# Performance work log

Hardware: AMD Instinct MI355X
Metric: run time of the kernel (lower is better)

The kernel has to match this reference:

```python
import jax, jax.numpy as jnp
import numpy as np

T, H, I, E, TOPK = 4096, 2880, 2880, 16, 4
EPS = 1e-5
ALPHA = 1.702


def setup_inputs() -> dict:
    key = jax.random.key(0)
    ks = jax.random.split(key, 8)
    s = 0.02
    return {
        "x": jax.random.normal(ks[0], (T, H), dtype=jnp.float32),
        "norm_w": jnp.ones((H,), dtype=jnp.float32),
        "gate_w": jax.random.normal(ks[1], (E, H), dtype=jnp.float32) * s,
        "gate_b": jax.random.normal(ks[2], (E,), dtype=jnp.float32) * s,
        "w1": jax.random.normal(ks[3], (E, 2 * I, H), dtype=jnp.float32) * s,  # fused gate_up
        "b1": jax.random.normal(ks[4], (E, 2 * I), dtype=jnp.float32) * s,
        "w2": jax.random.normal(ks[5], (E, H, I), dtype=jnp.float32) * s,      # down proj
        "b2": jax.random.normal(ks[6], (E, H), dtype=jnp.float32) * s,
    }


def _rmsnorm(x, w, eps=EPS):
    var = jnp.mean(x * x, axis=-1, keepdims=True)
    return x * jax.lax.rsqrt(var + eps) * w


def _swiglu(gu):
    glu, lin = jnp.split(gu, 2, axis=-1)
    return glu * jax.nn.sigmoid(ALPHA * glu) * (lin + 1.0)


def reference(x, norm_w, gate_w, gate_b, w1, b1, w2, b2):
    t = _rmsnorm(x, norm_w)                       # [T, H]
    logits = t @ gate_w.T + gate_b                # [T, E]
    # Renormalize routing: top-k of logits, softmax over the k selected logits
    vals, idx = jax.lax.top_k(logits, TOPK)       # [T, k]
    wts = jax.nn.softmax(vals, axis=-1)           # [T, k]
    combine = jnp.zeros((t.shape[0], E), dtype=t.dtype)
    combine = combine.at[jnp.arange(t.shape[0])[:, None], idx].set(wts)  # [T, E]
    out = jnp.zeros_like(x)
    for e in range(E):                            # small fixed expert loop
        gu = t @ w1[e].T + b1[e]                  # [T, 2I]
        y = _swiglu(gu) @ w2[e].T + b2[e]         # [T, H]
        out = out + combine[:, e:e + 1] * y
    return x + out
```

## Files before the change

### kernel.cpp

```cpp
#include <hip/hip_runtime.h>
#include <hip/hip_bf16.h>
#include <math.h>
#include <stdint.h>

#define T_TOK 4096
#define H_DIM 2880
#define E_NUM 16
#define ALPHA 1.702f
#define EPS_RMS 1e-5f

#define PADM 192
#define BK 32
#define NK (H_DIM / BK)
#define MAX_RT 104
#define NCT1 30
#define NCT2 15
#define G1 (MAX_RT * NCT1)
#define G2 (MAX_RT * NCT2)
#define ABUF 12288
#define BBUF 12288
#define BOFF 36864

typedef __attribute__((ext_vector_type(8))) short short8;
typedef __attribute__((ext_vector_type(4))) float f32x4;

__device__ __forceinline__ unsigned short f2bf(float f) {
  unsigned u = __float_as_uint(f);
  return (unsigned short)((u + 0x7fffu + ((u >> 16) & 1u)) >> 16);
}
__device__ __forceinline__ unsigned cpk(float a, float b) {
  unsigned r;
  asm("v_cvt_pk_bf16_f32 %0, %1, %2" : "=v"(r) : "v"(a), "v"(b));
  return r;
}
__device__ __forceinline__ void gl_lds16(const void* g, unsigned char* lds_dst) {
  __builtin_amdgcn_global_load_lds(
      (const __attribute__((address_space(1))) void*)g,
      (__attribute__((address_space(3))) void*)lds_dst, 16, 0, 0);
}
#define ENDSTEP() do {                                           \
    asm volatile("s_waitcnt lgkmcnt(0)" ::: "memory");           \
    __builtin_amdgcn_s_barrier();                                \
    __builtin_amdgcn_sched_barrier(0);                           \
  } while (0)

__global__ __launch_bounds__(256) void k_norm_gate(
    const float* __restrict__ x, const float* __restrict__ norm_w,
    const float* __restrict__ gate_w, const float* __restrict__ gate_b,
    float* __restrict__ out, unsigned short* __restrict__ t_out,
    int* __restrict__ topk_id, float* __restrict__ topk_w,
    int* __restrict__ counts)
{
  int t = blockIdx.x, tid = threadIdx.x;
  const float4* xr = (const float4*)(x + (size_t)t * H_DIM);
  float4* outr = (float4*)(out + (size_t)t * H_DIM);
  float4 xa[3];
  float ss = 0.f;
  int j = 0;
  for (int i = tid; i < 720; i += 256, j++) {
    float4 v = xr[i]; xa[j] = v; outr[i] = v;
    ss += v.x * v.x + v.y * v.y + v.z * v.z + v.w * v.w;
  }
#pragma unroll
  for (int o = 1; o < 64; o <<= 1) ss += __shfl_xor(ss, o, 64);
  __shared__ float red[4];
  if ((tid & 63) == 0) red[tid >> 6] = ss;
  __syncthreads();
  float rs = rsqrtf((red[0] + red[1] + red[2] + red[3]) * (1.f / H_DIM) + EPS_RMS);

  float part[16];
#pragma unroll
  for (int q = 0; q < 16; q++) part[q] = 0.f;
  j = 0;
  for (int i = tid; i < 720; i += 256, j++) {
    float4 v = xa[j];
    float4 w = ((const float4*)norm_w)[i];
    float t0 = v.x * rs * w.x, t1 = v.y * rs * w.y;
    float t2 = v.z * rs * w.z, t3 = v.w * rs * w.w;
    ushort4 b; b.x = f2bf(t0); b.y = f2bf(t1); b.z = f2bf(t2); b.w = f2bf(t3);
    ((ushort4*)(t_out + (size_t)t * H_DIM))[i] = b;
#pragma unroll
    for (int q = 0; q < 16; q++) {
      float4 g = ((const float4*)(gate_w + (size_t)q * H_DIM))[i];
      part[q] += t0 * g.x + t1 * g.y + t2 * g.z + t3 * g.w;
    }
  }
  __shared__ float lg[4][16];
#pragma unroll
  for (int q = 0; q < 16; q++) {
    float p = part[q];
#pragma unroll
    for (int o = 1; o < 64; o <<= 1) p += __shfl_xor(p, o, 64);
    if ((tid & 63) == 0) lg[tid >> 6][q] = p;
  }
  __syncthreads();
  if (tid == 0) {
    float logit[16];
    for (int q = 0; q < 16; q++)
      logit[q] = lg[0][q] + lg[1][q] + lg[2][q] + lg[3][q] + gate_b[q];
    unsigned used = 0; int idx[4]; float val[4];
    for (int k = 0; k < 4; k++) {
      float best = -3.4e38f; int bi = 0;
      for (int q = 0; q < 16; q++)
        if (!((used >> q) & 1u) && logit[q] > best) { best = logit[q]; bi = q; }
      used |= 1u << bi; idx[k] = bi; val[k] = best;
    }
    float s0 = 0.f, w4[4];
    for (int k = 0; k < 4; k++) { w4[k] = expf(val[k] - val[0]); s0 += w4[k]; }
    for (int k = 0; k < 4; k++) {
      topk_id[t * 4 + k] = idx[k];
      topk_w[t * 4 + k] = w4[k] / s0;
      atomicAdd(&counts[idx[k]], 1);
    }
  }
}

__global__ void k_offsets(const int* __restrict__ counts, int* __restrict__ d_off) {
  if (threadIdx.x == 0) {
    int acc = 0;
    for (int q = 0; q < 16; q++) {
      d_off[q] = acc;
      acc += ((counts[q] + PADM - 1) / PADM) * PADM;
    }
    d_off[16] = acc;
  }
}

__global__ __launch_bounds__(256) void k_fill(
    const int* __restrict__ topk_id, const float* __restrict__ topk_w,
    const int* __restrict__ counts, const int* __restrict__ d_off,
    int* __restrict__ perm_tok, float* __restrict__ perm_w)
{
  int e = blockIdx.x;
  int base = d_off[e], pe = d_off[e + 1] - base, cnt = counts[e];
  int tid = threadIdx.x, lane = tid & 63, wv = tid >> 6;
  __shared__ int wsum[4];
  int pos = 0;
  for (int c0 = 0; c0 < T_TOK; c0 += 256) {
    int tok = c0 + tid;
    int4 ids = ((const int4*)topk_id)[tok];
    int flag = 0, slot = 0;
    if (ids.x == e) { flag = 1; slot = 0; }
    else if (ids.y == e) { flag = 1; slot = 1; }
    else if (ids.z == e) { flag = 1; slot = 2; }
    else if (ids.w == e) { flag = 1; slot = 3; }
    unsigned long long b = __ballot(flag);
    int wprefix = __popcll(b & ((1ULL << lane) - 1ULL));
    if (lane == 0) wsum[wv] = __popcll(b);
    __syncthreads();
    int woff = 0;
    for (int i = 0; i < wv; i++) woff += wsum[i];
    int tot = wsum[0] + wsum[1] + wsum[2] + wsum[3];
    if (flag) {
      int p = base + pos + woff + wprefix;
      perm_tok[p] = tok;
      perm_w[p] = topk_w[tok * 4 + slot];
    }
    pos += tot;
    __syncthreads();
  }
  for (int i = cnt + tid; i < pe; i += 256) {
    perm_tok[base + i] = 0;
    perm_w[base + i] = 0.f;
  }
}

#define STAGE_A(abuf, ktn) do {                                               \
  _Pragma("unroll")                                                           \
  for (int i = 0; i < 3; i++)                                                 \
    gl_lds16(aptr[i] + (size_t)(ktn) * BK, lds + (abuf) * ABUF + adst[i]);    \
} while (0)

#define LOAD_B(ktn) do {                                                      \
  _Pragma("unroll")                                                           \
  for (int j = 0; j < 3; j++) {                                               \
    bv[j][0] = bptr[j][(ktn) * 8];                                            \
    bv[j][1] = bptr[j][(ktn) * 8 + 1];                                        \
  }                                                                           \
} while (0)

#define PACK_B(bbuf) do {                                                     \
  _Pragma("unroll")                                                           \
  for (int j = 0; j < 3; j++) {                                               \
    uint4 p;                                                                  \
    p.x = cpk(bv[j][0].x, bv[j][0].y); p.y = cpk(bv[j][0].z, bv[j][0].w);     \
    p.z = cpk(bv[j][1].x, bv[j][1].y); p.w = cpk(bv[j][1].z, bv[j][1].w);     \
    *(uint4*)(lds + BOFF + (bbuf) * BBUF + bdst[j]) = p;                      \
  }                                                                           \
} while (0)

#define COMPUTE(abuf, bbuf) do {                                              \
  const unsigned char* Abase = lds + (abuf) * ABUF + abase_off;               \
  const unsigned char* Bbase = lds + BOFF + (bbuf) * BBUF + bbase_off;        \
  short8 a0 = *(const short8*)(Abase);                                        \
  short8 a1 = *(const short8*)(Abase + 1024);                                 \
  short8 a2 = *(const short8*)(Abase + 2048);                                 \
  __builtin_amdgcn_s_setprio(1);                                              \
  _Pragma("unroll")                                                           \
  for (int n = 0; n < 12; n++) {                                              \
    short8 b = *(const short8*)(Bbase + n * 1024);                            \
    acc[0][n] = __builtin_amdgcn_mfma_f32_16x16x32_bf16(a0, b, acc[0][n], 0, 0, 0); \
    acc[1][n] = __builtin_amdgcn_mfma_f32_16x16x32_bf16(a1, b, acc[1][n], 0, 0, 0); \
    acc[2][n] = __builtin_amdgcn_mfma_f32_16x16x32_bf16(a2, b, acc[2][n], 0, 0, 0); \
  }                                                                           \
  __builtin_amdgcn_s_setprio(0);                                              \
} while (0)

#define GEMM_PIPE() do {                                                      \
  STAGE_A(0, 0); STAGE_A(1, 1); LOAD_B(0);                                    \
  PACK_B(0);                \
  ENDSTEP();                                                                  \
  int ca = 0;                                                                 \
  _Pragma("unroll 1")                                                         \
  for (int u = 0; u < NK / 2; u++) {                                          \
    int kt = 2 * u;                                                           \
    int ca1 = ca + 1; if (ca1 >= 3) ca1 -= 3;                                 \
    int ca2 = ca + 2; if (ca2 >= 3) ca2 -= 3;                                 \
    if (kt + 1 < NK) LOAD_B(kt + 1);                                          \
    if (kt + 2 < NK) STAGE_A(ca2, kt + 2);                                    \
    COMPUTE(ca, 0);                                                           \
    if (kt + 1 < NK) PACK_B(1);                                               \
    ENDSTEP();                                                                \
    if (kt + 2 < NK) LOAD_B(kt + 2);                                          \
    if (kt + 3 < NK) STAGE_A(ca, kt + 3);                                     \
    COMPUTE(ca1, 1);                                                          \
    if (kt + 2 < NK) PACK_B(0);                                               \
    ENDSTEP();                                                                \
    ca = ca2;                                                                 \
  }                                                                           \
} while (0)

__global__ __launch_bounds__(256, 2) void k_gemm1(
    const unsigned short* __restrict__ t_bf16,
    const float* __restrict__ w1, const float* __restrict__ b1,
    const int* __restrict__ perm_tok, const int* __restrict__ d_off,
    unsigned short* __restrict__ act)
{
  __shared__ __align__(16) unsigned char lds[3 * ABUF + 2 * BBUF];
  const int total = d_off[16];
  int bid = blockIdx.x;
  int wg = (bid & 7) * (G1 / 8) + (bid >> 3);
  int ct = wg / MAX_RT, rt = wg % MAX_RT;
  int rowbase = rt * PADM;
  if (rowbase >= total) return;
  int e = 0;
#pragma unroll
  for (int q = 0; q < E_NUM; q++) if (d_off[q + 1] <= rowbase) e = q + 1;

  int tid = threadIdx.x, lane = tid & 63, wv = tid >> 6;
  int lr = lane & 15, ch = lane >> 4;
  unsigned swz16 = (unsigned)((ch ^ ((lr >> 1) & 3)) << 4);
  unsigned abase_off = (unsigned)(wv * 3072 + lr * 64) + swz16;
  unsigned bbase_off = (unsigned)(lr * 64) + swz16;

  const unsigned short* aptr[3]; unsigned adst[3];
#pragma unroll
  for (int i = 0; i < 3; i++) {
    int cl = tid + 256 * i;
    int r = cl >> 2, c = cl & 3;
    int tok = perm_tok[rowbase + r];
    aptr[i] = t_bf16 + (size_t)tok * H_DIM + ((c ^ ((r >> 1) & 3)) * 8);
    adst[i] = (unsigned)cl * 16;
  }
  const float4* bptr[3]; unsigned bdst[3];
#pragma unroll
  for (int j = 0; j < 3; j++) {
    int idx = tid + 256 * j;
    int rr = idx >> 2, c = idx & 3;
    size_t grow = (size_t)e * (2 * H_DIM) +
                  (rr < 96 ? (size_t)(ct * 96 + rr) : (size_t)(H_DIM + ct * 96 + (rr - 96)));
    bptr[j] = (const float4*)(w1 + grow * H_DIM) + c * 2;
    bdst[j] = (unsigned)(rr * 64 + ((c ^ ((rr >> 1) & 3)) << 4));
  }

  f32x4 zero = {0.f, 0.f, 0.f, 0.f};
  f32x4 acc[3][12];
#pragma unroll
  for (int m = 0; m < 3; m++)
#pragma unroll
    for (int n = 0; n < 12; n++) acc[m][n] = zero;
  float4 bv[3][2];

  GEMM_PIPE();

  int rq = lane >> 4;
#pragma unroll
  for (int m = 0; m < 3; m++) {
    int row0 = rowbase + wv * 48 + m * 16 + rq * 4;
#pragma unroll
    for (int n = 0; n < 6; n++) {
      int col = ct * 96 + n * 16 + lr;
      float bg = b1[(size_t)e * (2 * H_DIM) + col];
      float bl = b1[(size_t)e * (2 * H_DIM) + H_DIM + col];
#pragma unroll
      for (int j = 0; j < 4; j++) {
        float g = acc[m][n][j] + bg;
        float l = acc[m][n + 6][j] + bl;
        float s = 1.f / (1.f + __expf(-ALPHA * g));
        act[(size_t)(row0 + j) * H_DIM + col] = f2bf(g * s * (l + 1.f));
      }
    }
  }
}

__global__ __launch_bounds__(256, 2) void k_gemm2(
    const unsigned short* __restrict__ act,
    const float* __restrict__ w2, const float* __restrict__ b2,
    const int* __restrict__ perm_tok, const float* __restrict__ perm_w,
    const int* __restrict__ d_off,
    float* __restrict__ out)
{
  __shared__ __align__(16) unsigned char lds[3 * ABUF + 2 * BBUF];
  __shared__ int stok[PADM]; __shared__ float swt[PADM];
  const int total = d_off[16];
  int bid = blockIdx.x;
  int wg = (bid & 7) * (G2 / 8) + (bid >> 3);
  int ct = wg / MAX_RT, rt = wg % MAX_RT;
  int rowbase = rt * PADM;
  if (rowbase >= total) return;
  int e = 0;
#pragma unroll
  for (int q = 0; q < E_NUM; q++) if (d_off[q + 1] <= rowbase) e = q + 1;

  int tid = threadIdx.x, lane = tid & 63, wv = tid >> 6;
  int lr = lane & 15, ch = lane >> 4;
  unsigned swz16 = (unsigned)((ch ^ ((lr >> 1) & 3)) << 4);
  unsigned abase_off = (unsigned)(wv * 3072 + lr * 64) + swz16;
  unsigned bbase_off = (unsigned)(lr * 64) + swz16;

  if (tid < PADM) { stok[tid] = perm_tok[rowbase + tid]; swt[tid] = perm_w[rowbase + tid]; }

  const unsigned short* aptr[3]; unsigned adst[3];
#pragma unroll
  for (int i = 0; i < 3; i++) {
    int cl = tid + 256 * i;
    int r = cl >> 2, c = cl & 3;
    aptr[i] = act + (size_t)(rowbase + r) * H_DIM + ((c ^ ((r >> 1) & 3)) * 8);
    adst[i] = (unsigned)cl * 16;
  }
  const float4* bptr[3]; unsigned bdst[3];
#pragma unroll
  for (int j = 0; j < 3; j++) {
    int idx = tid + 256 * j;
    int rr = idx >> 2, c = idx & 3;
    size_t grow = (size_t)e * H_DIM + (size_t)(ct * 192 + rr);
    bptr[j] = (const float4*)(w2 + grow * H_DIM) + c * 2;
    bdst[j] = (unsigned)(rr * 64 + ((c ^ ((rr >> 1) & 3)) << 4));
  }

  f32x4 zero = {0.f, 0.f, 0.f, 0.f};
  f32x4 acc[3][12];
#pragma unroll
  for (int m = 0; m < 3; m++)
#pragma unroll
    for (int n = 0; n < 12; n++) acc[m][n] = zero;
  float4 bv[3][2];

  GEMM_PIPE();

  int rq = lane >> 4;
#pragma unroll
  for (int m = 0; m < 3; m++) {
    int rl0 = wv * 48 + m * 16 + rq * 4;
#pragma unroll
    for (int n = 0; n < 12; n++) {
      int col = ct * 192 + n * 16 + lr;
      float b2v = b2[(size_t)e * H_DIM + col];
#pragma unroll
      for (int j = 0; j < 4; j++) {
        int rl = rl0 + j;
        float w = swt[rl];
        if (w != 0.f)
          atomicAdd(out + (size_t)stok[rl] * H_DIM + col, (acc[m][n][j] + b2v) * w);
      }
    }
  }
}

extern "C" void kernel_launch(void* const* d_in, const int* in_sizes, int n_in,
                              void* d_out, int out_size, void* d_ws, size_t ws_size,
                              hipStream_t stream)
{
  const float* x      = (const float*)d_in[0];
  const float* norm_w = (const float*)d_in[1];
  const float* gate_w = (const float*)d_in[2];
  const float* gate_b = (const float*)d_in[3];
  const float* w1     = (const float*)d_in[4];
  const float* b1     = (const float*)d_in[5];
  const float* w2     = (const float*)d_in[6];
  const float* b2     = (const float*)d_in[7];
  float* out = (float*)d_out;
  char* ws = (char*)d_ws;

  unsigned short* t_bf16  = (unsigned short*)(ws);
  unsigned short* act     = (unsigned short*)(ws + 23592960);
  int*            topk_id = (int*)(ws + 138608640);
  float*          topk_w  = (float*)(ws + 138674176);
  int*            perm_tk = (int*)(ws + 138739712);
  float*          perm_w  = (float*)(ws + 138819584);
  int*            counts  = (int*)(ws + 138899456);
  int*            d_off   = (int*)(ws + 138899520);

  hipMemsetAsync(counts, 0, 64, stream);
  hipLaunchKernelGGL(k_norm_gate, dim3(T_TOK), dim3(256), 0, stream,
                     x, norm_w, gate_w, gate_b, out, t_bf16, topk_id, topk_w, counts);
  hipLaunchKernelGGL(k_offsets, dim3(1), dim3(64), 0, stream, counts, d_off);
  hipLaunchKernelGGL(k_fill, dim3(16), dim3(256), 0, stream,
                     topk_id, topk_w, counts, d_off, perm_tk, perm_w);
  hipLaunchKernelGGL(k_gemm1, dim3(G1), dim3(256), 0, stream,
                     t_bf16, w1, b1, perm_tk, d_off, act);
  hipLaunchKernelGGL(k_gemm2, dim3(G2), dim3(256), 0, stream,
                     act, w2, b2, perm_tk, perm_w, d_off, out);
}
```

Measured before the change: 1.573 ms.

## Triple-buffer B tile in LDS and deepen weight prefetch pipeline

Restructures the GEMM main loop so the B (weight) tile gets three LDS buffers like A, unrolled by three steps. Global B loads are now issued two k-steps ahead, and a sched_barrier separates the MFMA compute from the bf16 pack/store. The aim is to hide more of the fp32 weight-load latency behind the MFMAs. In exchange it uses more LDS per block (five to six 12 KB buffers), which may limit occupancy, and keeps B registers live longer.

After: 5.945 ms. 278% more time.

```diff
diff --git a/kernel.cpp b/kernel.cpp
--- a/kernel.cpp
+++ b/kernel.cpp
@@ -189,9 +189,9 @@
   }                                                                           \
 } while (0)
 
-#define COMPUTE(abuf, bbuf) do {                                              \
-  const unsigned char* Abase = lds + (abuf) * ABUF + abase_off;               \
-  const unsigned char* Bbase = lds + BOFF + (bbuf) * BBUF + bbase_off;        \
+#define COMPUTE(cb) do {                                                      \
+  const unsigned char* Abase = lds + (cb) * ABUF + abase_off;                 \
+  const unsigned char* Bbase = lds + BOFF + (cb) * BBUF + bbase_off;          \
   short8 a0 = *(const short8*)(Abase);                                        \
   short8 a1 = *(const short8*)(Abase + 1024);                                 \
   short8 a2 = *(const short8*)(Abase + 2048);                                 \
@@ -206,27 +206,28 @@
   __builtin_amdgcn_s_setprio(0);                                              \
 } while (0)
 
+#define GEMM_STEP(kt, CB, PB) do {                                            \
+    if ((kt) + 2 < NK) STAGE_A(PB, (kt) + 2);                                 \
+    COMPUTE(CB);                                                              \
+    __builtin_amdgcn_sched_barrier(0);                                        \
+    if ((kt) + 2 < NK) PACK_B(PB);                                            \
+    else asm volatile("s_waitcnt vmcnt(0)" ::: "memory");                     \
+    if ((kt) + 3 < NK) LOAD_B((kt) + 3);                                      \
+    ENDSTEP();                                                                \
+  } while (0)
+
 #define GEMM_PIPE() do {                                                      \
-  STAGE_A(0, 0); STAGE_A(1, 1); LOAD_B(0);                                    \
-  PACK_B(0);                \
+  STAGE_A(0, 0); STAGE_A(1, 1);                                               \
+  LOAD_B(0); PACK_B(0);                                                       \
+  LOAD_B(1); PACK_B(1);     \
+  LOAD_B(2);                             \
   ENDSTEP();                                                                  \
-  int ca = 0;                                                                 \
   _Pragma("unroll 1")                                                         \
-  for (int u = 0; u < NK / 2; u++) {                                          \
-    int kt = 2 * u;                                                           \
-    int ca1 = ca + 1; if (ca1 >= 3) ca1 -= 3;                                 \
-    int ca2 = ca + 2; if (ca2 >= 3) ca2 -= 3;                                 \
-    if (kt + 1 < NK) LOAD_B(kt + 1);                                          \
-    if (kt + 2 < NK) STAGE_A(ca2, kt + 2);                                    \
-    COMPUTE(ca, 0);                                                           \
-    if (kt + 1 < NK) PACK_B(1);                                               \
-    ENDSTEP();                                                                \
-    if (kt + 2 < NK) LOAD_B(kt + 2);                                          \
-    if (kt + 3 < NK) STAGE_A(ca, kt + 3);                                     \
-    COMPUTE(ca1, 1);                                                          \
-    if (kt + 2 < NK) PACK_B(0);                                               \
-    ENDSTEP();                                                                \
-    ca = ca2;                                                                 \
+  for (int u = 0; u < NK / 3; u++) {                                          \
+    int kt = 3 * u;                                                           \
+    GEMM_STEP(kt,     0, 2);                                                  \
+    GEMM_STEP(kt + 1, 1, 0);                                                  \
+    GEMM_STEP(kt + 2, 2, 1);                                                  \
   }                                                                           \
 } while (0)
 
@@ -236,7 +237,7 @@
     const int* __restrict__ perm_tok, const int* __restrict__ d_off,
     unsigned short* __restrict__ act)
 {
-  __shared__ __align__(16) unsigned char lds[3 * ABUF + 2 * BBUF];
+  __shared__ __align__(16) unsigned char lds[3 * ABUF + 3 * BBUF];
   const int total = d_off[16];
   int bid = blockIdx.x;
   int wg = (bid & 7) * (G1 / 8) + (bid >> 3);
@@ -310,7 +311,7 @@
     const int* __restrict__ d_off,
     float* __restrict__ out)
 {
-  __shared__ __align__(16) unsigned char lds[3 * ABUF + 2 * BBUF];
+  __shared__ __align__(16) unsigned char lds[3 * ABUF + 3 * BBUF];
   __shared__ int stok[PADM]; __shared__ float swt[PADM];
   const int total = d_off[16];
   int bid = blockIdx.x;
```

## Pre-convert expert weights to bf16 and use async LDS-staged GEMMs when workspace allows

Applied to the files above, without the earlier changes.

Adds a conversion kernel that writes w1 and w2 to bf16 in the workspace before each expert GEMM. New GEMM kernels stage both A and B tiles into LDS asynchronously in a three-buffer pipeline, with a 2x2 wave tiling over 6x3 or 6x6 fragments. This removes the per-thread fp32 weight loads and register packing. The cost is an extra full pass over the fp32 weights, writing 2-byte copies, on every call. The new path runs only if the workspace is large enough; otherwise the old kernels run, with slightly reordered staging.

After: 2.858 ms. +81.7%, slower.

```diff
diff --git a/kernel.cpp b/kernel.cpp
--- a/kernel.cpp
+++ b/kernel.cpp
@@ -165,6 +165,21 @@
   }
 }
 
+__global__ __launch_bounds__(256) void k_cvt(
+    const float* __restrict__ src, unsigned short* __restrict__ dst, int n8)
+{
+  int i = blockIdx.x * 256 + threadIdx.x;
+  int stride = gridDim.x * 256;
+  for (; i < n8; i += stride) {
+    float4 a = ((const float4*)src)[2 * i];
+    float4 b = ((const float4*)src)[2 * i + 1];
+    uint4 o;
+    o.x = cpk(a.x, a.y); o.y = cpk(a.z, a.w);
+    o.z = cpk(b.x, b.y); o.w = cpk(b.z, b.w);
+    ((uint4*)dst)[i] = o;
+  }
+}
+
 #define STAGE_A(abuf, ktn) do {                                               \
   _Pragma("unroll")                                                           \
   for (int i = 0; i < 3; i++)                                                 \
@@ -206,9 +221,17 @@
   __builtin_amdgcn_s_setprio(0);                                              \
 } while (0)
 
-#define GEMM_PIPE() do {                                                      \
+#define GEMM_STEP_F(kt, CB, PB) do {                                          \
+    if ((kt) + 1 < NK) LOAD_B((kt) + 1);                                      \
+    if ((kt) + 2 < NK) STAGE_A(PB, (kt) + 2);                                 \
+    COMPUTE(CB, (kt) & 1);                                                    \
+    if ((kt) + 1 < NK) PACK_B(((kt) + 1) & 1);                                \
+    ENDSTEP();                                                                \
+  } while (0)
+
+#define GEMM_PIPE_F() do {                                                    \
   STAGE_A(0, 0); STAGE_A(1, 1); LOAD_B(0);                                    \
-  PACK_B(0);                \
+  PACK_B(0);                                                                  \
   ENDSTEP();                                                                  \
   int ca = 0;                                                                 \
   _Pragma("unroll 1")                                                         \
@@ -216,13 +239,13 @@
     int kt = 2 * u;                                                           \
     int ca1 = ca + 1; if (ca1 >= 3) ca1 -= 3;                                 \
     int ca2 = ca + 2; if (ca2 >= 3) ca2 -= 3;                                 \
+    if (kt + 2 < NK) STAGE_A(ca2, kt + 2);                                    \
     if (kt + 1 < NK) LOAD_B(kt + 1);                                          \
-    if (kt + 2 < NK) STAGE_A(ca2, kt + 2);                                    \
     COMPUTE(ca, 0);                                                           \
     if (kt + 1 < NK) PACK_B(1);                                               \
     ENDSTEP();                                                                \
+    if (kt + 3 < NK) STAGE_A(ca, kt + 3);                                     \
     if (kt + 2 < NK) LOAD_B(kt + 2);                                          \
-    if (kt + 3 < NK) STAGE_A(ca, kt + 3);                                     \
     COMPUTE(ca1, 1);                                                          \
     if (kt + 2 < NK) PACK_B(0);                                               \
     ENDSTEP();                                                                \
@@ -230,7 +253,7 @@
   }                                                                           \
 } while (0)
 
-__global__ __launch_bounds__(256, 2) void k_gemm1(
+__global__ __launch_bounds__(256, 2) void k_gemm1_f(
     const unsigned short* __restrict__ t_bf16,
     const float* __restrict__ w1, const float* __restrict__ b1,
     const int* __restrict__ perm_tok, const int* __restrict__ d_off,
@@ -281,7 +304,7 @@
     for (int n = 0; n < 12; n++) acc[m][n] = zero;
   float4 bv[3][2];
 
-  GEMM_PIPE();
+  GEMM_PIPE_F();
 
   int rq = lane >> 4;
 #pragma unroll
@@ -303,7 +326,7 @@
   }
 }
 
-__global__ __launch_bounds__(256, 2) void k_gemm2(
+__global__ __launch_bounds__(256, 2) void k_gemm2_f(
     const unsigned short* __restrict__ act,
     const float* __restrict__ w2, const float* __restrict__ b2,
     const int* __restrict__ perm_tok, const float* __restrict__ perm_w,
@@ -356,7 +379,7 @@
     for (int n = 0; n < 12; n++) acc[m][n] = zero;
   float4 bv[3][2];
 
-  GEMM_PIPE();
+  GEMM_PIPE_F();
 
   int rq = lane >> 4;
 #pragma unroll
@@ -372,6 +395,211 @@
         float w = swt[rl];
         if (w != 0.f)
           atomicAdd(out + (size_t)stok[rl] * H_DIM + col, (acc[m][n][j] + b2v) * w);
+      }
+    }
+  }
+}
+
+#define STAGE_BW(bbuf, ktn) do {                                              \
+  _Pragma("unroll")                                                           \
+  for (int i = 0; i < 3; i++)                                                 \
+    gl_lds16(bpt[i] + (size_t)(ktn) * BK, lds + BOFF + (bbuf) * BBUF + adst[i]); \
+} while (0)
+
+#define WWAIT(full) do {                                                      \
+    if (full) asm volatile("s_waitcnt vmcnt(6)" ::: "memory");                \
+    else      asm volatile("s_waitcnt vmcnt(0)" ::: "memory");                \
+    __builtin_amdgcn_sched_barrier(0);                                        \
+    __builtin_amdgcn_s_barrier();                                             \
+    __builtin_amdgcn_sched_barrier(0);                                        \
+  } while (0)
+
+#define WSTEP(kt, CB, SB, COMP) do {                                          \
+    if ((kt) + 2 < NK) { STAGE_A(SB, (kt) + 2); STAGE_BW(SB, (kt) + 2); }     \
+    COMP(CB);                                                                 \
+    if ((kt) + 1 < NK) WWAIT((kt) + 2 < NK);                                  \
+  } while (0)
+
+#define WPIPE(COMP) do {                                                      \
+  STAGE_A(0, 0); STAGE_BW(0, 0);                                              \
+  STAGE_A(1, 1); STAGE_BW(1, 1);                                              \
+  WWAIT(1);                                                                   \
+  _Pragma("unroll 1")                                                         \
+  for (int u = 0; u < NK / 3; u++) {                                          \
+    int kt = 3 * u;                                                           \
+    WSTEP(kt,     0, 2, COMP);                                                \
+    WSTEP(kt + 1, 1, 0, COMP);                                                \
+    WSTEP(kt + 2, 2, 1, COMP);                                                \
+  }                                                                           \
+} while (0)
+
+#define COMP_G1(cb) do {                                                      \
+  const unsigned char* Ab = lds + (cb) * ABUF;                                \
+  const unsigned char* Bb = lds + BOFF + (cb) * BBUF;                         \
+  short8 a_[6];                                                               \
+  _Pragma("unroll")                                                           \
+  for (int mf = 0; mf < 6; mf++) a_[mf] = *(const short8*)(Ab + abase + mf * 1024); \
+  __builtin_amdgcn_s_setprio(1);                                              \
+  _Pragma("unroll")                                                           \
+  for (int nf = 0; nf < 3; nf++) {                                            \
+    short8 bg = *(const short8*)(Bb + bgbase + nf * 1024);                    \
+    short8 bl = *(const short8*)(Bb + blbase + nf * 1024);                    \
+    _Pragma("unroll")                                                         \
+    for (int mf = 0; mf < 6; mf++) {                                          \
+      accg[mf][nf] = __builtin_amdgcn_mfma_f32_16x16x32_bf16(a_[mf], bg, accg[mf][nf], 0, 0, 0); \
+      accl[mf][nf] = __builtin_amdgcn_mfma_f32_16x16x32_bf16(a_[mf], bl, accl[mf][nf], 0, 0, 0); \
+    }                                                                         \
+  }                                                                           \
+  __builtin_amdgcn_s_setprio(0);                                              \
+} while (0)
+
+#define COMP_G2(cb) do {                                                      \
+  const unsigned char* Ab = lds + (cb) * ABUF;                                \
+  const unsigned char* Bb = lds + BOFF + (cb) * BBUF;                         \
+  short8 a_[6];                                                               \
+  _Pragma("unroll")                                                           \
+  for (int mf = 0; mf < 6; mf++) a_[mf] = *(const short8*)(Ab + abase + mf * 1024); \
+  __builtin_amdgcn_s_setprio(1);                                              \
+  _Pragma("unroll")                                                           \
+  for (int nf = 0; nf < 6; nf++) {                                            \
+    short8 b = *(const short8*)(Bb + bbase + nf * 1024);                      \
+    _Pragma("unroll")                                                         \
+    for (int mf = 0; mf < 6; mf++)                                            \
+      acc[mf][nf] = __builtin_amdgcn_mfma_f32_16x16x32_bf16(a_[mf], b, acc[mf][nf], 0, 0, 0); \
+  }                                                                           \
+  __builtin_amdgcn_s_setprio(0);                                              \
+} while (0)
+
+__global__ __launch_bounds__(256, 2) void k_gemm1_w(
+    const unsigned short* __restrict__ t_bf16,
+    const unsigned short* __restrict__ w1b, const float* __restrict__ b1,
+    const int* __restrict__ perm_tok, const int* __restrict__ d_off,
+    unsigned short* __restrict__ act)
+{
+  __shared__ __align__(16) unsigned char lds[3 * ABUF + 3 * BBUF];
+  const int total = d_off[16];
+  int bid = blockIdx.x;
+  int wg = (bid & 7) * (G1 / 8) + (bid >> 3);
+  int ct = wg / MAX_RT, rt = wg % MAX_RT;
+  int rowbase = rt * PADM;
+  if (rowbase >= total) return;
+  int e = 0;
+#pragma unroll
+  for (int q = 0; q < E_NUM; q++) if (d_off[q + 1] <= rowbase) e = q + 1;
+
+  int tid = threadIdx.x, lane = tid & 63, wv = tid >> 6;
+  int wr = wv & 1, wc = wv >> 1;
+  int lr = lane & 15, ch = lane >> 4;
+  unsigned swz16 = (unsigned)((ch ^ ((lr >> 1) & 3)) << 4);
+  unsigned abase  = (unsigned)((wr * 96 + lr) * 64) + swz16;
+  unsigned bgbase = (unsigned)((wc * 48 + lr) * 64) + swz16;
+  unsigned blbase = bgbase + 96 * 64;
+
+  const unsigned short* aptr[3]; const unsigned short* bpt[3]; unsigned adst[3];
+#pragma unroll
+  for (int i = 0; i < 3; i++) {
+    int cl = tid + 256 * i;
+    int r = cl >> 2, c = cl & 3;
+    int cs = (c ^ ((r >> 1) & 3)) * 8;
+    int tok = perm_tok[rowbase + r];
+    aptr[i] = t_bf16 + (size_t)tok * H_DIM + cs;
+    size_t grow = (size_t)e * (2 * H_DIM) +
+                  (r < 96 ? (size_t)(ct * 96 + r) : (size_t)(H_DIM + ct * 96 + (r - 96)));
+    bpt[i] = w1b + grow * H_DIM + cs;
+    adst[i] = (unsigned)cl * 16;
+  }
+
+  f32x4 zero = {0.f, 0.f, 0.f, 0.f};
+  f32x4 accg[6][3], accl[6][3];
+#pragma unroll
+  for (int m = 0; m < 6; m++)
+#pragma unroll
+    for (int n = 0; n < 3; n++) { accg[m][n] = zero; accl[m][n] = zero; }
+
+  WPIPE(COMP_G1);
+
+  int rq = lane >> 4;
+#pragma unroll
+  for (int mf = 0; mf < 6; mf++) {
+    int row0 = rowbase + wr * 96 + mf * 16 + rq * 4;
+#pragma unroll
+    for (int nf = 0; nf < 3; nf++) {
+      int col = ct * 96 + wc * 48 + nf * 16 + lr;
+      float bg = b1[(size_t)e * (2 * H_DIM) + col];
+      float bl = b1[(size_t)e * (2 * H_DIM) + H_DIM + col];
+#pragma unroll
+      for (int j = 0; j < 4; j++) {
+        float g = accg[mf][nf][j] + bg;
+        float l = accl[mf][nf][j] + bl;
+        float s = 1.f / (1.f + __expf(-ALPHA * g));
+        act[(size_t)(row0 + j) * H_DIM + col] = f2bf(g * s * (l + 1.f));
+      }
+    }
+  }
+}
+
+__global__ __launch_bounds__(256, 2) void k_gemm2_w(
+    const unsigned short* __restrict__ act,
+    const unsigned short* __restrict__ w2b, const float* __restrict__ b2,
+    const int* __restrict__ perm_tok, const float* __restrict__ perm_w,
+    const int* __restrict__ d_off,
+    float* __restrict__ out)
+{
+  __shared__ __align__(16) unsigned char lds[3 * ABUF + 3 * BBUF];
+  __shared__ int stok[PADM]; __shared__ float swt[PADM];
+  const int total = d_off[16];
+  int bid = blockIdx.x;
+  int wg = (bid & 7) * (G2 / 8) + (bid >> 3);
+  int ct = wg / MAX_RT, rt = wg % MAX_RT;
+  int rowbase = rt * PADM;
+  if (rowbase >= total) return;
+  int e = 0;
+#pragma unroll
+  for (int q = 0; q < E_NUM; q++) if (d_off[q + 1] <= rowbase) e = q + 1;
+
+  int tid = threadIdx.x, lane = tid & 63, wv = tid >> 6;
+  int wr = wv & 1, wc = wv >> 1;
+  int lr = lane & 15, ch = lane >> 4;
+  unsigned swz16 = (unsigned)((ch ^ ((lr >> 1) & 3)) << 4);
+  unsigned abase = (unsigned)((wr * 96 + lr) * 64) + swz16;
+  unsigned bbase = (unsigned)((wc * 96 + lr) * 64) + swz16;
+
+  if (tid < PADM) { stok[tid] = perm_tok[rowbase + tid]; swt[tid] = perm_w[rowbase + tid]; }
+
+  const unsigned short* aptr[3]; const unsigned short* bpt[3]; unsigned adst[3];
+#pragma unroll
+  for (int i = 0; i < 3; i++) {
+    int cl = tid + 256 * i;
+    int r = cl >> 2, c = cl & 3;
+    int cs = (c ^ ((r >> 1) & 3)) * 8;
+    aptr[i] = act + (size_t)(rowbase + r) * H_DIM + cs;
+    bpt[i] = w2b + ((size_t)e * H_DIM + (size_t)(ct * 192 + r)) * H_DIM + cs;
+    adst[i] = (unsigned)cl * 16;
+  }
+
+  f32x4 zero = {0.f, 0.f, 0.f, 0.f};
+  f32x4 acc[6][6];
+#pragma unroll
+  for (int m = 0; m < 6; m++)
+#pragma unroll
+    for (int n = 0; n < 6; n++) acc[m][n] = zero;
+
+  WPIPE(COMP_G2);
+
+  int rq = lane >> 4;
+#pragma unroll
+  for (int mf = 0; mf < 6; mf++) {
+    int rl0 = wr * 96 + mf * 16 + rq * 4;
+#pragma unroll
+    for (int nf = 0; nf < 6; nf++) {
+      int col = ct * 192 + wc * 96 + nf * 16 + lr;
+      float b2v = b2[(size_t)e * H_DIM + col];
+#pragma unroll
+      for (int j = 0; j < 4; j++) {
+        int rl = rl0 + j;
+        float w = swt[rl];
+        if (w != 0.f)
+          atomicAdd(out + (size_t)stok[rl] * H_DIM + col, (acc[mf][nf][j] + b2v) * w);
       }
     }
   }
@@ -400,6 +628,9 @@
   float*          perm_w  = (float*)(ws + 138819584);
   int*            counts  = (int*)(ws + 138899456);
   int*            d_off   = (int*)(ws + 138899520);
+  unsigned short* wb      = (unsigned short*)(ws + 138900480);
+  const size_t NEED = 138900480ULL + 132710400ULL;
+  bool bigws = ws_size >= NEED;
 
   hipMemsetAsync(counts, 0, 64, stream);
   hipLaunchKernelGGL(k_norm_gate, dim3(T_TOK), dim3(256), 0, stream,
@@ -407,8 +638,17 @@
   hipLaunchKernelGGL(k_offsets, dim3(1), dim3(64), 0, stream, counts, d_off);
   hipLaunchKernelGGL(k_fill, dim3(16), dim3(256), 0, stream,
                      topk_id, topk_w, counts, d_off, perm_tk, perm_w);
-  hipLaunchKernelGGL(k_gemm1, dim3(G1), dim3(256), 0, stream,
-                     t_bf16, w1, b1, perm_tk, d_off, act);
-  hipLaunchKernelGGL(k_gemm2, dim3(G2), dim3(256), 0, stream,
-                     act, w2, b2, perm_tk, perm_w, d_off, out);
-}
+  if (bigws) {
+    hipLaunchKernelGGL(k_cvt, dim3(2048), dim3(256), 0, stream, w1, wb, 33177600);
+    hipLaunchKernelGGL(k_gemm1_w, dim3(G1), dim3(256), 0, stream,
+                       t_bf16, wb, b1, perm_tk, d_off, act);
+    hipLaunchKernelGGL(k_cvt, dim3(2048), dim3(256), 0, stream, w2, wb, 16588800);
+    hipLaunchKernelGGL(k_gemm2_w, dim3(G2), dim3(256), 0, stream,
+                       act, wb, b2, perm_tk, perm_w, d_off, out);
+  } else {
+    hipLaunchKernelGGL(k_gemm1_f, dim3(G1), dim3(256), 0, stream,
+                       t_bf16, w1, b1, perm_tk, d_off, act);
+    hipLaunchKernelGGL(k_gemm2_f, dim3(G2), dim3(256), 0, stream,
+                       act, w2, b2, perm_tk, perm_w, d_off, out);
+  }
+}
```

## Replace fp32 atomic scatter with per-slot bf16 outputs and a combine kernel

Applied to the files above, without the earlier changes.

The down-projection epilogue no longer does fp32 atomicAdd into the output. Each routed row now writes its weighted result as bf16 into a per-top-k-slot buffer, indexed by a new slot id array built in k_fill. A new k_comb kernel adds x and the four slot buffers into the output, which removes the residual copy from k_norm_gate and all atomic contention. The cost is an extra launch, about 94MB of bf16 intermediate traffic, and bf16 rounding of each expert contribution before summation.

New measurement: 1.489 ms. 5.3% less time.

```diff
diff --git a/kernel.cpp b/kernel.cpp
--- a/kernel.cpp
+++ b/kernel.cpp
@@ -33,6 +33,9 @@
   asm("v_cvt_pk_bf16_f32 %0, %1, %2" : "=v"(r) : "v"(a), "v"(b));
   return r;
 }
+__device__ __forceinline__ float bf2f(unsigned short s) {
+  return __uint_as_float((unsigned)s << 16);
+}
 __device__ __forceinline__ void gl_lds16(const void* g, unsigned char* lds_dst) {
   __builtin_amdgcn_global_load_lds(
       (const __attribute__((address_space(1))) void*)g,
@@ -47,18 +50,17 @@
 __global__ __launch_bounds__(256) void k_norm_gate(
     const float* __restrict__ x, const float* __restrict__ norm_w,
     const float* __restrict__ gate_w, const float* __restrict__ gate_b,
-    float* __restrict__ out, unsigned short* __restrict__ t_out,
+    unsigned short* __restrict__ t_out,
     int* __restrict__ topk_id, float* __restrict__ topk_w,
     int* __restrict__ counts)
 {
   int t = blockIdx.x, tid = threadIdx.x;
   const float4* xr = (const float4*)(x + (size_t)t * H_DIM);
-  float4* outr = (float4*)(out + (size_t)t * H_DIM);
   float4 xa[3];
   float ss = 0.f;
   int j = 0;
   for (int i = tid; i < 720; i += 256, j++) {
-    float4 v = xr[i]; xa[j] = v; outr[i] = v;
+    float4 v = xr[i]; xa[j] = v;
     ss += v.x * v.x + v.y * v.y + v.z * v.z + v.w * v.w;
   }
 #pragma unroll
@@ -129,7 +131,8 @@
 __global__ __launch_bounds__(256) void k_fill(
     const int* __restrict__ topk_id, const float* __restrict__ topk_w,
     const int* __restrict__ counts, const int* __restrict__ d_off,
-    int* __restrict__ perm_tok, float* __restrict__ perm_w)
+    int* __restrict__ perm_tok, float* __restrict__ perm_w,
+    int* __restrict__ perm_sl)
 {
   int e = blockIdx.x;
   int base = d_off[e], pe = d_off[e + 1] - base, cnt = counts[e];
@@ -155,13 +158,15 @@
       int p = base + pos + woff + wprefix;
       perm_tok[p] = tok;
       perm_w[p] = topk_w[tok * 4 + slot];
+      perm_sl[p] = slot;
     }
     pos += tot;
     __syncthreads();
   }
   for (int i = cnt + tid; i < pe; i += 256) {
-    perm_tok[base + i] = 0;
+    perm_tok[base + i] = -1;
     perm_w[base + i] = 0.f;
+    perm_sl[base + i] = 0;
   }
 }
 
@@ -208,7 +213,7 @@
 
 #define GEMM_PIPE() do {                                                      \
   STAGE_A(0, 0); STAGE_A(1, 1); LOAD_B(0);                                    \
-  PACK_B(0);                \
+  PACK_B(0);                                                                  \
   ENDSTEP();                                                                  \
   int ca = 0;                                                                 \
   _Pragma("unroll 1")                                                         \
@@ -259,6 +264,7 @@
     int cl = tid + 256 * i;
     int r = cl >> 2, c = cl & 3;
     int tok = perm_tok[rowbase + r];
+    if (tok < 0) tok = 0;
     aptr[i] = t_bf16 + (size_t)tok * H_DIM + ((c ^ ((r >> 1) & 3)) * 8);
     adst[i] = (unsigned)cl * 16;
   }
@@ -307,11 +313,11 @@
     const unsigned short* __restrict__ act,
     const float* __restrict__ w2, const float* __restrict__ b2,
     const int* __restrict__ perm_tok, const float* __restrict__ perm_w,
-    const int* __restrict__ d_off,
-    float* __restrict__ out)
+    const int* __restrict__ perm_sl, const int* __restrict__ d_off,
+    unsigned short* __restrict__ yslot)
 {
   __shared__ __align__(16) unsigned char lds[3 * ABUF + 2 * BBUF];
-  __shared__ int stok[PADM]; __shared__ float swt[PADM];
+  __shared__ int stok[PADM]; __shared__ float swt[PADM]; __shared__ int ssl[PADM];
   const int total = d_off[16];
   int bid = blockIdx.x;
   int wg = (bid & 7) * (G2 / 8) + (bid >> 3);
@@ -328,7 +334,11 @@
   unsigned abase_off = (unsigned)(wv * 3072 + lr * 64) + swz16;
   unsigned bbase_off = (unsigned)(lr * 64) + swz16;
 
-  if (tid < PADM) { stok[tid] = perm_tok[rowbase + tid]; swt[tid] = perm_w[rowbase + tid]; }
+  if (tid < PADM) {
+    stok[tid] = perm_tok[rowbase + tid];
+    swt[tid] = perm_w[rowbase + tid];
+    ssl[tid] = perm_sl[rowbase + tid];
+  }
 
   const unsigned short* aptr[3]; unsigned adst[3];
 #pragma unroll
@@ -369,11 +379,41 @@
 #pragma unroll
       for (int j = 0; j < 4; j++) {
         int rl = rl0 + j;
-        float w = swt[rl];
-        if (w != 0.f)
-          atomicAdd(out + (size_t)stok[rl] * H_DIM + col, (acc[m][n][j] + b2v) * w);
+        int tk = stok[rl];
+        if (tk >= 0) {
+          float y = (acc[m][n][j] + b2v) * swt[rl];
+          yslot[((size_t)ssl[rl] * T_TOK + tk) * H_DIM + col] = f2bf(y);
+        }
       }
     }
+  }
+}
+
+__global__ __launch_bounds__(256) void k_comb(
+    const float* __restrict__ x, const unsigned short* __restrict__ yslot,
+    float* __restrict__ out)
+{
+  const int n8 = T_TOK * H_DIM / 8;
+  int i = blockIdx.x * 256 + threadIdx.x;
+  int stride = gridDim.x * 256;
+  for (; i < n8; i += stride) {
+    float4 x0 = ((const float4*)x)[2 * i];
+    float4 x1 = ((const float4*)x)[2 * i + 1];
+    float s[8] = {x0.x, x0.y, x0.z, x0.w, x1.x, x1.y, x1.z, x1.w};
+#pragma unroll
+    for (int k = 0; k < 4; k++) {
+      uint4 v = ((const uint4*)(yslot + (size_t)k * T_TOK * H_DIM))[i];
+      unsigned u[4] = {v.x, v.y, v.z, v.w};
+#pragma unroll
+      for (int q = 0; q < 4; q++) {
+        s[2 * q]     += __uint_as_float(u[q] << 16);
+        s[2 * q + 1] += __uint_as_float(u[q] & 0xffff0000u);
+      }
+    }
+    float4 o0 = {s[0], s[1], s[2], s[3]};
+    float4 o1 = {s[4], s[5], s[6], s[7]};
+    ((float4*)out)[2 * i] = o0;
+    ((float4*)out)[2 * i + 1] = o1;
   }
 }
 
@@ -398,17 +438,20 @@
   float*          topk_w  = (float*)(ws + 138674176);
   int*            perm_tk = (int*)(ws + 138739712);
   float*          perm_w  = (float*)(ws + 138819584);
-  int*            counts  = (int*)(ws + 138899456);
-  int*            d_off   = (int*)(ws + 138899520);
+  int*            perm_sl = (int*)(ws + 138899456);
+  int*            counts  = (int*)(ws + 138979328);
+  int*            d_off   = (int*)(ws + 138979392);
+  unsigned short* yslot   = (unsigned short*)(ws + 138979840);
 
   hipMemsetAsync(counts, 0, 64, stream);
   hipLaunchKernelGGL(k_norm_gate, dim3(T_TOK), dim3(256), 0, stream,
-                     x, norm_w, gate_w, gate_b, out, t_bf16, topk_id, topk_w, counts);
+                     x, norm_w, gate_w, gate_b, t_bf16, topk_id, topk_w, counts);
   hipLaunchKernelGGL(k_offsets, dim3(1), dim3(64), 0, stream, counts, d_off);
   hipLaunchKernelGGL(k_fill, dim3(16), dim3(256), 0, stream,
-                     topk_id, topk_w, counts, d_off, perm_tk, perm_w);
+                     topk_id, topk_w, counts, d_off, perm_tk, perm_w, perm_sl);
   hipLaunchKernelGGL(k_gemm1, dim3(G1), dim3(256), 0, stream,
                      t_bf16, w1, b1, perm_tk, d_off, act);
   hipLaunchKernelGGL(k_gemm2, dim3(G2), dim3(256), 0, stream,
-                     act, w2, b2, perm_tk, perm_w, d_off, out);
-}
+                     act, w2, b2, perm_tk, perm_w, perm_sl, d_off, yslot);
+  hipLaunchKernelGGL(k_comb, dim3(2048), dim3(256), 0, stream, x, yslot, out);
+}
```
